# Performance work log

Hardware: AMD Instinct MI355X
Metric: run time of the kernel (lower is better)

Reference implementation:

```python
import jax, jax.numpy as jnp
import numpy as np

N = 20000          # cells (graph nodes)
E = 320000         # edges (avg degree 16)
IN, MID, OUT = 2, 128, 3
HEADS = (4, 4, 1)
CONCAT = (False, False, True)
BN_EPS = 1e-5


def setup_inputs() -> dict:
    key = jax.random.key(0)
    ks = jax.random.split(key, 40)
    f32 = jnp.float32
    inp = {
        "x": jax.random.normal(ks[0], (N, IN), f32),
        "edge_index": jax.random.randint(ks[1], (2, E), 0, N, jnp.int32),
        "gene_index": 0,
    }
    in_dims = (IN, MID, MID)
    out_dims = (MID, MID, OUT)
    i = 2
    for L in range(3):
        H, C = HEADS[L], out_dims[L]
        inp[f"W{L}"] = jax.random.normal(ks[i], (H * C, in_dims[L]), f32) * 0.1; i += 1
        inp[f"as{L}"] = jax.random.normal(ks[i], (H, C), f32) * 0.1; i += 1
        inp[f"ad{L}"] = jax.random.normal(ks[i], (H, C), f32) * 0.1; i += 1
        bdim = H * C if CONCAT[L] else C
        inp[f"b{L}"] = jax.random.normal(ks[i], (bdim,), f32) * 0.1; i += 1
    for L in range(2):
        inp[f"bn_g{L}"] = 1.0 + jax.random.normal(ks[i], (MID,), f32) * 0.1; i += 1
        inp[f"bn_b{L}"] = jax.random.normal(ks[i], (MID,), f32) * 0.1; i += 1
        inp[f"bn_m{L}"] = jax.random.normal(ks[i], (MID,), f32) * 0.1; i += 1
        inp[f"bn_v{L}"] = jax.random.uniform(ks[i], (MID,), f32, minval=0.5, maxval=1.5); i += 1
    inp["k"] = jax.random.normal(ks[i], (1,), f32); i += 1
    inp["d"] = jax.random.normal(ks[i], (1,), f32) * 0.1; i += 1
    inp["t0"] = jax.random.uniform(ks[i], (1,), f32) * 0.2; i += 1
    inp["u0"] = jax.random.uniform(ks[i], (1,), f32); i += 1
    inp["t"] = jax.random.uniform(ks[i], (N, 1), f32); i += 1
    return inp


def _gat(x, W, a_s, a_d, b, src, dst, heads, concat):
    # PyG GATConv (eval): linear -> per-node head scores -> edge leaky_relu
    # -> segment softmax over dst -> scatter-weighted aggregate -> bias.
    n = x.shape[0]
    h = (x @ W.T).reshape(n, heads, -1)                      # [N,H,C]
    logit = jax.nn.leaky_relu(
        (h * a_s).sum(-1)[src] + (h * a_d).sum(-1)[dst], 0.2)  # [E,H]
    m = jax.ops.segment_max(logit, dst, num_segments=n)
    p = jnp.exp(logit - m[dst])
    alpha = p / (jax.ops.segment_sum(p, dst, num_segments=n)[dst] + 1e-16)
    out = jax.ops.segment_sum(h[src] * alpha[:, :, None], dst, num_segments=n)
    out = out.reshape(n, -1) if concat else out.mean(axis=1)
    return out + b


def _forward(x, edge_index, gene_index,
             W0, as0, ad0, b0, W1, as1, ad1, b1, W2, as2, ad2, b2,
             bn_g0, bn_b0, bn_m0, bn_v0, bn_g1, bn_b1, bn_m1, bn_v1,
             k, d, t0, u0, t):
    n = x.shape[0]
    loop = jnp.arange(n, dtype=edge_index.dtype)             # add_self_loops=True
    src = jnp.concatenate([edge_index[0], loop])
    dst = jnp.concatenate([edge_index[1], loop])
    convs = ((W0, as0, ad0, b0), (W1, as1, ad1, b1), (W2, as2, ad2, b2))
    bns = ((bn_g0, bn_b0, bn_m0, bn_v0), (bn_g1, bn_b1, bn_m1, bn_v1))
    for L in range(3):
        W, a_s, a_d, b = convs[L]
        x = jax.nn.elu(_gat(x, W, a_s, a_d, b, src, dst, HEADS[L], CONCAT[L]))
        if L != 2:
            g_, b_, m_, v_ = bns[L]
            x = (x - m_) * jax.lax.rsqrt(v_ + BN_EPS) * g_ + b_   # BN eval
            # dropout is a no-op in eval mode
    a_r = x[:, 0]
    gam = x[:, 1]
    bet = x[:, 2]
    g = gene_index
    tt = t[:, g]
    S = jax.nn.sigmoid(k[g] * (tt - t0[g] - d[g]))
    eb = jnp.exp(-bet * tt)
    eg = jnp.exp(-gam * tt)
    ebs = jnp.exp(-bet * (tt - t0[g]))
    egs = jnp.exp(-gam * (tt - t0[g]))
    ab = a_r / bet
    ag = a_r / gam
    tilde_u = ab * (1 - eb) * (1 - S) + ab * S + (u0[g] * ebs - ab) * S
    tilde_s = (ag * (1 - eg) + a_r / (gam - bet) * (eg - eb)) * (1 - S) \
              + ag * S + bet * u0[g] / (gam - bet) * (egs - ebs) * S
    return tilde_u, tilde_s


def reference(x, edge_index, gene_index,
              W0, as0, ad0, b0, W1, as1, ad1, b1, W2, as2, ad2, b2,
              bn_g0, bn_b0, bn_m0, bn_v0, bn_g1, bn_b1, bn_m1, bn_v1,
              k, d, t0, u0, t):
    return _forward(x, edge_index, gene_index,
                    W0, as0, ad0, b0, W1, as1, ad1, b1, W2, as2, ad2, b2,
                    bn_g0, bn_b0, bn_m0, bn_v0, bn_g1, bn_b1, bn_m1, bn_v1,
                    k, d, t0, u0, t)
```

## Files before the change

### kernel.cpp

```cpp
#include <hip/hip_runtime.h>
#include <hip/hip_bf16.h>

#define CAP 64

typedef __attribute__((ext_vector_type(8))) short bf16x8;
typedef __attribute__((ext_vector_type(4))) float f32x4;

__device__ __forceinline__ float eluf(float x){ return x > 0.f ? x : expm1f(x); }
__device__ __forceinline__ float lrelu(float x){ return x >= 0.f ? x : 0.2f*x; }

__device__ __forceinline__ float ldf(const void* p, size_t i, int f){
  if(f) return ((const float*)p)[i];
  unsigned u = ((const unsigned short*)p)[i];
  return __uint_as_float(u << 16);
}

__device__ __forceinline__ unsigned pk2(float a, float b){
  __hip_bfloat16 ba = __float2bfloat16(a), bb = __float2bfloat16(b);
  unsigned short ua = *(unsigned short*)&ba, ub = *(unsigned short*)&bb;
  return (unsigned)ua | ((unsigned)ub << 16);
}
__device__ __forceinline__ float lo16(unsigned u){ return __uint_as_float(u << 16); }
__device__ __forceinline__ float hi16(unsigned u){ return __uint_as_float(u & 0xffff0000u); }

__device__ __forceinline__ float4 shfl4(float4 v, int m){
  return make_float4(__shfl_xor(v.x,m), __shfl_xor(v.y,m), __shfl_xor(v.z,m), __shfl_xor(v.w,m));
}
__device__ __forceinline__ float4 add4(float4 a, float4 b){
  return make_float4(a.x+b.x, a.y+b.y, a.z+b.z, a.w+b.w);
}

__global__ void zero_detect(const unsigned short* __restrict__ w1raw, int* __restrict__ flag,
                            int* __restrict__ cursor, int N){
  int i = blockIdx.x*256 + threadIdx.x;
  if(i < N) cursor[i] = 0;
  if(blockIdx.x == 0){
    __shared__ int cnt;
    if(threadIdx.x == 0) cnt = 0;
    __syncthreads();
    int c = 0;
    for(int k = threadIdx.x; k < 2048; k += 256){
      unsigned int u = w1raw[2*k];
      float v = __uint_as_float(u << 16);
      if(fabsf(v) > 100.f) c++;
    }
    atomicAdd(&cnt, c);
    __syncthreads();
    if(threadIdx.x == 0) *flag = (cnt > 10) ? 1 : 0;
  }
}

#define NSEG 21
struct CvtDesc {
  const void* src[NSEG];
  float*      dst[NSEG];
  int         n[NSEG];
};
struct POff { int o[26]; };

__global__ void prep(CvtDesc cd, POff po, const int* __restrict__ flag,
    const void* __restrict__ W0r, const void* __restrict__ as0r, const void* __restrict__ ad0r,
    const void* __restrict__ W1r, const void* __restrict__ as1r, const void* __restrict__ ad1r,
    unsigned short* __restrict__ Wgb, float* __restrict__ W1sa, float* __restrict__ W1da,
    float* __restrict__ W0sa, float* __restrict__ W0da,
    const int* __restrict__ ei, int E, int N,
    int* __restrict__ cursor, int* __restrict__ csr){
  int bid = blockIdx.x, t = threadIdx.x;
  int sec = 0;
  while(sec < 24 && bid >= po.o[sec+1]) sec++;
  int lb = bid - po.o[sec];
  int f = *flag;
  if(sec < NSEG){
    int i = lb*256 + t;
    if(i < cd.n[sec]) cd.dst[sec][i] = ldf(cd.src[sec], i, f);
  } else if(sec == NSEG){
    int id = lb*256 + t;
    if(id < 512*128){
      int c = id >> 9, m = id & 511;
      int h = m >> 7, k = m & 127;
      float v = ldf(W1r, (size_t)(h*128 + c)*128 + k, f);
      __hip_bfloat16 bv = __float2bfloat16(v);
      Wgb[id] = *(unsigned short*)&bv;
    }
  } else if(sec == NSEG+1){
    int e = lb*256 + t, Et = E + N;
    if(e < Et){
      int s, d;
      if(e < E){ s = ei[e]; d = ei[E + e]; } else { s = d = e - E; }
      int pos = atomicAdd(&cursor[d], 1);
      if(pos < CAP) csr[(size_t)d*CAP + pos] = s;
    }
  } else if(sec == NSEG+2){
    int gw = (lb*256 + t) >> 6;
    int lane = t & 63;
    int h = gw & 3, w = gw >> 2;
    const void* A = w ? ad1r : as1r;
    float sk0 = 0.f, sk1 = 0.f;
    for(int c = 0; c < 128; c++){
      float a = ldf(A, h*128 + c, f);
      size_t ro = (size_t)(h*128 + c)*128;
      sk0 += ldf(W1r, ro + lane,      f) * a;
      sk1 += ldf(W1r, ro + lane + 64, f) * a;
    }
    float* D = w ? W1da : W1sa;
    D[lane*4 + h]        = sk0;
    D[(lane + 64)*4 + h] = sk1;
  } else {
    int idx = lb*256 + t;
    if(idx < 16){
      int col = idx & 1, h = (idx >> 1) & 3, w = idx >> 3;
      const void* A = w ? ad0r : as0r;
      float s = 0.f;
      for(int c = 0; c < 128; c++)
        s += ldf(W0r, (size_t)(h*128+c)*2 + col, f) * ldf(A, h*128+c, f);
      (w ? W0da : W0sa)[h*2 + col] = s;
    }
  }
}

__global__ __launch_bounds__(256) void gather0(
    const int* __restrict__ cursor, const int* __restrict__ csr,
    const float* __restrict__ xf,
    const float* __restrict__ W0f,
    const float* __restrict__ W0sa, const float* __restrict__ W0da,
    const float* __restrict__ W1sa, const float* __restrict__ W1da,
    const float* __restrict__ b0,
    const float* __restrict__ bn_g, const float* __restrict__ bn_b,
    const float* __restrict__ bn_m, const float* __restrict__ bn_v,
    unsigned* __restrict__ x1b,
    float* __restrict__ ssrc, float* __restrict__ sdst){
  int t = threadIdx.x, wv = t >> 6, lane = t & 63;
  int hh = lane >> 5, l32 = lane & 31;
  int n = blockIdx.x*8 + wv*2 + hh;
  int cnt = min(cursor[n], CAP);
  float2 xn = ((const float2*)xf)[n];
  float4 sd4;
  sd4.x = xn.x*W0da[0] + xn.y*W0da[1];
  sd4.y = xn.x*W0da[2] + xn.y*W0da[3];
  sd4.z = xn.x*W0da[4] + xn.y*W0da[5];
  sd4.w = xn.x*W0da[6] + xn.y*W0da[7];
  float2 xs0 = make_float2(0.f,0.f), xs1 = make_float2(0.f,0.f);
  float4 p0 = make_float4(0.f,0.f,0.f,0.f), p1 = make_float4(0.f,0.f,0.f,0.f);
  if(l32 < cnt){
    int src = csr[(size_t)n*CAP + l32];
    xs0 = ((const float2*)xf)[src];
    p0.x = expf(lrelu(xs0.x*W0sa[0] + xs0.y*W0sa[1] + sd4.x));
    p0.y = expf(lrelu(xs0.x*W0sa[2] + xs0.y*W0sa[3] + sd4.y));
    p0.z = expf(lrelu(xs0.x*W0sa[4] + xs0.y*W0sa[5] + sd4.z));
    p0.w = expf(lrelu(xs0.x*W0sa[6] + xs0.y*W0sa[7] + sd4.w));
  }
  if(l32 + 32 < cnt){
    int src = csr[(size_t)n*CAP + l32 + 32];
    xs1 = ((const float2*)xf)[src];
    p1.x = expf(lrelu(xs1.x*W0sa[0] + xs1.y*W0sa[1] + sd4.x));
    p1.y = expf(lrelu(xs1.x*W0sa[2] + xs1.y*W0sa[3] + sd4.y));
    p1.z = expf(lrelu(xs1.x*W0sa[4] + xs1.y*W0sa[5] + sd4.z));
    p1.w = expf(lrelu(xs1.x*W0sa[6] + xs1.y*W0sa[7] + sd4.w));
  }
  float4 dn = add4(p0, p1);
  #pragma unroll
  for(int o = 1; o < 32; o <<= 1) dn = add4(dn, shfl4(dn, o));
  float4 ax = make_float4(p0.x*xs0.x + p1.x*xs1.x, p0.y*xs0.x + p1.y*xs1.x,
                          p0.z*xs0.x + p1.z*xs1.x, p0.w*xs0.x + p1.w*xs1.x);
  float4 ay = make_float4(p0.x*xs0.y + p1.x*xs1.y, p0.y*xs0.y + p1.y*xs1.y,
                          p0.z*xs0.y + p1.z*xs1.y, p0.w*xs0.y + p1.w*xs1.y);
  #pragma unroll
  for(int o = 1; o < 32; o <<= 1){ ax = add4(ax, shfl4(ax, o)); ay = add4(ay, shfl4(ay, o)); }
  float4 inv;
  inv.x = 1.f/(dn.x + 1e-16f); inv.y = 1.f/(dn.y + 1e-16f);
  inv.z = 1.f/(dn.z + 1e-16f); inv.w = 1.f/(dn.w + 1e-16f);
  ax.x *= inv.x; ax.y *= inv.y; ax.z *= inv.z; ax.w *= inv.w;
  ay.x *= inv.x; ay.y *= inv.y; ay.z *= inv.z; ay.w *= inv.w;
  float o4[4];
  #pragma unroll
  for(int i = 0; i < 4; i++){
    int c = 4*l32 + i;
    float acc = W0f[(c      )*2]*ax.x + W0f[(c      )*2+1]*ay.x
              + W0f[(128 + c)*2]*ax.y + W0f[(128 + c)*2+1]*ay.y
              + W0f[(256 + c)*2]*ax.z + W0f[(256 + c)*2+1]*ay.z
              + W0f[(384 + c)*2]*ax.w + W0f[(384 + c)*2+1]*ay.w;
    float v = 0.25f*acc + b0[c];
    v = eluf(v);
    float sc = bn_g[c] * rsqrtf(bn_v[c] + 1e-5f);
    o4[i] = (v - bn_m[c])*sc + bn_b[c];
  }
  uint2 pk; pk.x = pk2(o4[0], o4[1]); pk.y = pk2(o4[2], o4[3]);
  ((uint2*)(x1b + (size_t)n*64))[l32] = pk;
  float4 ps = make_float4(0.f,0.f,0.f,0.f), pd = make_float4(0.f,0.f,0.f,0.f);
  #pragma unroll
  for(int i = 0; i < 4; i++){
    int c = 4*l32 + i;
    float4 ws = ((const float4*)W1sa)[c];
    float4 wd = ((const float4*)W1da)[c];
    ps.x += o4[i]*ws.x; ps.y += o4[i]*ws.y; ps.z += o4[i]*ws.z; ps.w += o4[i]*ws.w;
    pd.x += o4[i]*wd.x; pd.y += o4[i]*wd.y; pd.z += o4[i]*wd.z; pd.w += o4[i]*wd.w;
  }
  #pragma unroll
  for(int o = 1; o < 32; o <<= 1){ ps = add4(ps, shfl4(ps, o)); pd = add4(pd, shfl4(pd, o)); }
  if(l32 == 0){
    ((float4*)ssrc)[n] = ps;
    ((float4*)sdst)[n] = pd;
  }
}

__global__ __launch_bounds__(256) void agg1(
    const int* __restrict__ cursor, const int* __restrict__ csr,
    const float* __restrict__ s_src, const float* __restrict__ s_dst,
    const unsigned* __restrict__ x1b,
    unsigned* __restrict__ sAgg){
  __shared__ float lal[4][2][CAP*4];
  __shared__ int   lsr[4][2][CAP];
  int t = threadIdx.x, wv = t >> 6, lane = t & 63;
  int hh = lane >> 5, l32 = lane & 31;
  int n = blockIdx.x*8 + wv*2 + hh;
  int cnt = min(cursor[n], CAP);
  float4 sd4 = ((const float4*)s_dst)[n];
  float4 p0 = make_float4(0.f,0.f,0.f,0.f), p1 = make_float4(0.f,0.f,0.f,0.f);
  if(l32 < cnt){
    int src = csr[(size_t)n*CAP + l32];
    lsr[wv][hh][l32] = src;
    float4 ss4 = ((const float4*)s_src)[src];
    p0.x = expf(lrelu(ss4.x + sd4.x)); p0.y = expf(lrelu(ss4.y + sd4.y));
    p0.z = expf(lrelu(ss4.z + sd4.z)); p0.w = expf(lrelu(ss4.w + sd4.w));
    ((float4*)lal[wv][hh])[l32] = p0;
  }
  if(l32 + 32 < cnt){
    int src = csr[(size_t)n*CAP + l32 + 32];
    lsr[wv][hh][l32 + 32] = src;
    float4 ss4 = ((const float4*)s_src)[src];
    p1.x = expf(lrelu(ss4.x + sd4.x)); p1.y = expf(lrelu(ss4.y + sd4.y));
    p1.z = expf(lrelu(ss4.z + sd4.z)); p1.w = expf(lrelu(ss4.w + sd4.w));
    ((float4*)lal[wv][hh])[l32 + 32] = p1;
  }
  float4 dn = add4(p0, p1);
  #pragma unroll
  for(int o = 1; o < 32; o <<= 1) dn = add4(dn, shfl4(dn, o));
  float4 inv;
  inv.x = 1.f/(dn.x + 1e-16f); inv.y = 1.f/(dn.y + 1e-16f);
  inv.z = 1.f/(dn.z + 1e-16f); inv.w = 1.f/(dn.w + 1e-16f);
  float a0[4] = {0,0,0,0}, a1[4] = {0,0,0,0};
  float a2[4] = {0,0,0,0}, a3[4] = {0,0,0,0};
  const float4* alp = (const float4*)lal[wv][hh];
  const int* srcs = lsr[wv][hh];
  #pragma unroll 2
  for(int j = 0; j < cnt; j++){
    int src = srcs[j];
    uint2 uv = ((const uint2*)(x1b + (size_t)src*64))[l32];
    float4 al = alp[j];
    float c0 = lo16(uv.x), c1 = hi16(uv.x);
    float c2 = lo16(uv.y), c3 = hi16(uv.y);
    a0[0] += al.x*c0; a1[0] += al.x*c1; a2[0] += al.x*c2; a3[0] += al.x*c3;
    a0[1] += al.y*c0; a1[1] += al.y*c1; a2[1] += al.y*c2; a3[1] += al.y*c3;
    a0[2] += al.z*c0; a1[2] += al.z*c1; a2[2] += al.z*c2; a3[2] += al.z*c3;
    a0[3] += al.w*c0; a1[3] += al.w*c1; a2[3] += al.w*c2; a3[3] += al.w*c3;
  }
  float iv[4] = {inv.x, inv.y, inv.z, inv.w};
  uint2* out2 = (uint2*)(sAgg + (size_t)n*256);
  #pragma unroll
  for(int h = 0; h < 4; h++){
    uint2 pkv;
    pkv.x = pk2(a0[h]*iv[h], a1[h]*iv[h]);
    pkv.y = pk2(a2[h]*iv[h], a3[h]*iv[h]);
    out2[h*32 + l32] = pkv;
  }
}

__global__ __launch_bounds__(256) void gemm12_mfma(
    const unsigned short* __restrict__ sAgg16,
    const unsigned short* __restrict__ Wgb,
    const float* __restrict__ b1,
    const float* __restrict__ bn_g, const float* __restrict__ bn_b,
    const float* __restrict__ bn_m, const float* __restrict__ bn_v,
    const float* __restrict__ W2f,
    const float* __restrict__ as2f, const float* __restrict__ ad2f,
    float* __restrict__ h2, float* __restrict__ s_src, float* __restrict__ s_dst, int N){
  __shared__ float x2s[64][128];
  int t = threadIdx.x, wv = t >> 6, lane = t & 63;
  int col = lane & 15, quad = lane >> 4;
  int base = blockIdx.x*64;
  const unsigned short* arow = sAgg16 + (size_t)(base + wv*16 + col)*512;
  f32x4 acc[8];
  #pragma unroll
  for(int tc = 0; tc < 8; tc++) acc[tc] = (f32x4){0.f,0.f,0.f,0.f};
  for(int kk = 0; kk < 16; kk++){
    bf16x8 av = *(const bf16x8*)(arow + kk*32 + quad*8);
    #pragma unroll
    for(int tc = 0; tc < 8; tc++){
      bf16x8 bv = *(const bf16x8*)(Wgb + (size_t)(tc*16 + col)*512 + kk*32 + quad*8);
      acc[tc] = __builtin_amdgcn_mfma_f32_16x16x32_bf16(av, bv, acc[tc], 0, 0, 0);
    }
  }
  #pragma unroll
  for(int tc = 0; tc < 8; tc++){
    int ch = tc*16 + col;
    float sc = bn_g[ch] * rsqrtf(bn_v[ch] + 1e-5f);
    float mc = bn_m[ch], ob = bn_b[ch], bb = b1[ch];
    #pragma unroll
    for(int r = 0; r < 4; r++){
      int nl = wv*16 + quad*4 + r;
      float v = eluf(0.25f*acc[tc][r] + bb);
      x2s[nl][ch] = (v - mc)*sc + ob;
    }
  }
  __syncthreads();
  int nd = t >> 2, q = t & 3;
  int n = base + nd;
  const float* xr = x2s[nd];
  float c0 = 0.f, c1 = 0.f, cv2 = 0.f;
  for(int qq = q; qq < 32; qq += 4){
    float4 xv = *(const float4*)&xr[qq*4];
    float4 w0 = ((const float4*)(W2f      ))[qq];
    float4 w1 = ((const float4*)(W2f + 128))[qq];
    float4 w2 = ((const float4*)(W2f + 256))[qq];
    c0  += xv.x*w0.x + xv.y*w0.y + xv.z*w0.z + xv.w*w0.w;
    c1  += xv.x*w1.x + xv.y*w1.y + xv.z*w1.z + xv.w*w1.w;
    cv2 += xv.x*w2.x + xv.y*w2.y + xv.z*w2.z + xv.w*w2.w;
  }
  c0  += __shfl_xor(c0, 1);  c0  += __shfl_xor(c0, 2);
  c1  += __shfl_xor(c1, 1);  c1  += __shfl_xor(c1, 2);
  cv2 += __shfl_xor(cv2, 1); cv2 += __shfl_xor(cv2, 2);
  if(q == 0 && n < N){
    ((float4*)h2)[n] = make_float4(c0, c1, cv2, 0.f);
    s_src[n] = c0*as2f[0] + c1*as2f[1] + cv2*as2f[2];
    s_dst[n] = c0*ad2f[0] + c1*ad2f[1] + cv2*ad2f[2];
  }
}

__global__ __launch_bounds__(256) void gather_ode(const int* __restrict__ cursor,
    const int* __restrict__ csr,
    const float* __restrict__ s_src, const float* __restrict__ s_dst,
    const float* __restrict__ h2, const float* __restrict__ b2f,
    const float* __restrict__ scal,
    const float* __restrict__ tf, float* __restrict__ out, int N){
  int t = threadIdx.x, wv = t >> 6, lane = t & 63;
  int hh = lane >> 5, l32 = lane & 31;
  int n = blockIdx.x*8 + wv*2 + hh;
  int cnt = min(cursor[n], CAP);
  const int* row = csr + (size_t)n*CAP;
  float sd = s_dst[n];
  float pw0 = 0.f, pw1 = 0.f;
  float4 hv0 = make_float4(0,0,0,0), hv1 = make_float4(0,0,0,0);
  if(l32 < cnt){
    int s = row[l32];
    pw0 = expf(lrelu(s_src[s] + sd));
    hv0 = ((const float4*)h2)[s];
  }
  if(l32 + 32 < cnt){
    int s = row[l32 + 32];
    pw1 = expf(lrelu(s_src[s] + sd));
    hv1 = ((const float4*)h2)[s];
  }
  float den = pw0 + pw1;
  float a0 = pw0*hv0.x + pw1*hv1.x;
  float a1 = pw0*hv0.y + pw1*hv1.y;
  float a2 = pw0*hv0.z + pw1*hv1.z;
  #pragma unroll
  for(int o = 1; o < 32; o <<= 1){
    den += __shfl_xor(den, o);
    a0  += __shfl_xor(a0, o);
    a1  += __shfl_xor(a1, o);
    a2  += __shfl_xor(a2, o);
  }
  if(l32 != 0) return;
  double inv = 1.0/((double)den + 1e-16);
  double A0 = (double)a0*inv + (double)b2f[0];
  double A1 = (double)a1*inv + (double)b2f[1];
  double A2 = (double)a2*inv + (double)b2f[2];
  double ar  = A0 > 0.0 ? A0 : expm1(A0);
  double gam = A1 > 0.0 ? A1 : expm1(A1);
  double bet = A2 > 0.0 ? A2 : expm1(A2);
  double tt = (double)tf[n];
  double k = (double)scal[0], d = (double)scal[1];
  double t0 = (double)scal[2], u0 = (double)scal[3];
  double S = 1.0/(1.0 + exp(-(k*(tt - t0 - d))));
  double eb  = exp(-bet*tt),        eg  = exp(-gam*tt);
  double ebs = exp(-bet*(tt - t0)), egs = exp(-gam*(tt - t0));
  double ab = ar/bet, ag = ar/gam;
  double tu = ab*(1.0 - eb)*(1.0 - S) + ab*S + (u0*ebs - ab)*S;
  double gmb = gam - bet;
  double ts = (ag*(1.0 - eg) + ar/gmb*(eg - eb))*(1.0 - S) + ag*S
            + bet*u0/gmb*(egs - ebs)*S;
  out[n]     = (float)tu;
  out[N + n] = (float)ts;
}

extern "C" void kernel_launch(void* const* d_in, const int* in_sizes, int n_in,
                              void* d_out, int out_size, void* d_ws, size_t ws_size,
                              hipStream_t stream) {
  const int* ei = (const int*)d_in[1];
  int N = in_sizes[0] / 2;
  int E = in_sizes[1] / 2;
  int Et = E + N;

  char* ws = (char*)d_ws;
  size_t off = 0;
  auto alloc = [&](size_t bytes)->void*{
    void* p = ws + off; off += (bytes + 255) & ~(size_t)255; return p;
  };
  int*   flag  = (int*)  alloc(4);
  float* xf    = (float*)alloc((size_t)N*2*4);
  float* W0f   = (float*)alloc(1024*4);
  float* b0f   = (float*)alloc(128*4);
  float* b1f   = (float*)alloc(128*4);
  float* W2f   = (float*)alloc(384*4);
  float* as2f  = (float*)alloc(3*4);
  float* ad2f  = (float*)alloc(3*4);
  float* b2f   = (float*)alloc(3*4);
  float* bnf[8];
  for(int i = 0; i < 8; i++) bnf[i] = (float*)alloc(128*4);
  float* scal  = (float*)alloc(4*4);
  float* tf    = (float*)alloc((size_t)N*4);
  unsigned short* Wgb = (unsigned short*)alloc(65536*2);
  float* W1sa  = (float*)alloc(512*4);
  float* W1da  = (float*)alloc(512*4);
  float* W0sa  = (float*)alloc(8*4);
  float* W0da  = (float*)alloc(8*4);
  int*   cursor= (int*)  alloc((size_t)N*4);
  int*   csr   = (int*)  alloc((size_t)N*CAP*4);
  unsigned* x1b= (unsigned*)alloc((size_t)N*64*4);
  unsigned* sAgg=(unsigned*)alloc((size_t)(N + 64)*256*4);
  float* h2    = (float*)alloc((size_t)N*4*4);
  float* ssrc  = (float*)alloc((size_t)N*4*4);
  float* sdst  = (float*)alloc((size_t)N*4*4);

  zero_detect<<<(N + 255)/256, 256, 0, stream>>>((const unsigned short*)d_in[7], flag, cursor, N);

  CvtDesc cd;
  const int src_idx[NSEG] = {0,3,6,10, 11,12,13,14, 15,16,17,18,19,20,21,22, 23,24,25,26, 27};
  float* dsts[NSEG] = {xf,W0f,b0f,b1f, W2f,as2f,ad2f,b2f,
                       bnf[0],bnf[1],bnf[2],bnf[3],bnf[4],bnf[5],bnf[6],bnf[7],
                       scal+0,scal+1,scal+2,scal+3, tf};
  for(int i = 0; i < NSEG; i++){
    cd.src[i] = d_in[src_idx[i]];
    cd.dst[i] = dsts[i];
    cd.n[i]   = in_sizes[src_idx[i]];
  }
  POff po;
  int acc = 0;
  for(int i = 0; i < NSEG; i++){ po.o[i] = acc; acc += (cd.n[i] + 255)/256; }
  po.o[NSEG] = acc;   acc += 256;
  po.o[NSEG+1] = acc; acc += (Et + 255)/256;
  po.o[NSEG+2] = acc; acc += 2;
  po.o[NSEG+3] = acc; acc += 1;
  po.o[NSEG+4] = acc;
  prep<<<acc, 256, 0, stream>>>(cd, po, flag,
      d_in[3], d_in[4], d_in[5], d_in[7], d_in[8], d_in[9],
      Wgb, W1sa, W1da, W0sa, W0da, ei, E, N, cursor, csr);

  gather0<<<N/8, 256, 0, stream>>>(cursor, csr, xf, W0f, W0sa, W0da, W1sa, W1da, b0f,
                                   bnf[0], bnf[1], bnf[2], bnf[3], x1b, ssrc, sdst);
  agg1<<<N/8, 256, 0, stream>>>(cursor, csr, ssrc, sdst, x1b, sAgg);
  gemm12_mfma<<<(N + 63)/64, 256, 0, stream>>>((const unsigned short*)sAgg, Wgb,
                                   b1f, bnf[4], bnf[5], bnf[6], bnf[7],
                                   W2f, as2f, ad2f, h2, ssrc, sdst, N);
  gather_ode<<<N/8, 256, 0, stream>>>(cursor, csr, ssrc, sdst,
                                      h2, b2f, scal, tf,
                                      (float*)d_out, N);
}
```

Before: 247.5 us.

## Fuse all stages into one cooperative persistent kernel with grid syncs

Merges zero/detect, prep, gather0, agg1, gemm12 and gather_ode into a single cooperative kernel that loops over work with grid-stride loops and separates stages with grid-wide syncs. The goal is to remove per-launch overhead and the idle gaps between six dependent launches. The old multi-kernel path stays as a fallback if the cooperative launch fails. In exchange, the grid is capped by occupancy, so the persistent blocks loop over several node groups, and grid syncs carry their own cost. The large union shared buffer may also limit how many blocks fit per CU.

```diff
diff --git a/kernel.cpp b/kernel.cpp
--- a/kernel.cpp
+++ b/kernel.cpp
@@ -1,5 +1,8 @@
 #include <hip/hip_runtime.h>
 #include <hip/hip_bf16.h>
+#include <hip/hip_cooperative_groups.h>
+
+namespace cg = cooperative_groups;
 
 #define CAP 64
 
@@ -28,6 +31,355 @@
 }
 __device__ __forceinline__ float4 add4(float4 a, float4 b){
   return make_float4(a.x+b.x, a.y+b.y, a.z+b.z, a.w+b.w);
+}
+
+#define NSEG 21
+struct CvtDesc {
+  const void* src[NSEG];
+  float*      dst[NSEG];
+  int         n[NSEG];
+};
+struct POff { int o[26]; };
+
+struct MegaArgs {
+  CvtDesc cd; POff po;
+  const unsigned short* w1raw;
+  int* flag; int* cursor; int* csr;
+  const void *W0r, *as0r, *ad0r, *W1r, *as1r, *ad1r;
+  unsigned short* Wgb;
+  float *W1sa, *W1da, *W0sa, *W0da;
+  const int* ei;
+  float *xf, *W0f, *b0f, *b1f, *W2f, *as2f, *ad2f, *b2f;
+  float *bn0g, *bn0b, *bn0m, *bn0v, *bn1g, *bn1b, *bn1m, *bn1v;
+  float *scal, *tf;
+  unsigned *x1b, *sAgg;
+  float *h2, *ssrc, *sdst, *out;
+  int N, E, prep_total;
+};
+
+__global__ __launch_bounds__(256, 4) void mega(MegaArgs a){
+  __shared__ union SM {
+    struct { float lal[4][2][CAP*4]; int lsr[4][2][CAP]; } ag;
+    float x2s[64][128];
+    int cnt;
+  } sm;
+  cg::grid_group gg = cg::this_grid();
+  int t = threadIdx.x, wv = t >> 6, lane = t & 63;
+  int hh = lane >> 5, l32 = lane & 31;
+  int N = a.N, E = a.E;
+
+  for(int i = blockIdx.x*256 + t; i < N; i += gridDim.x*256) a.cursor[i] = 0;
+  if(blockIdx.x == 0){
+    if(t == 0) sm.cnt = 0;
+    __syncthreads();
+    int c = 0;
+    for(int k = t; k < 2048; k += 256){
+      unsigned u = a.w1raw[2*k];
+      float v = __uint_as_float(u << 16);
+      if(fabsf(v) > 100.f) c++;
+    }
+    atomicAdd(&sm.cnt, c);
+    __syncthreads();
+    if(t == 0) *a.flag = (sm.cnt > 10) ? 1 : 0;
+  }
+  gg.sync();
+
+  {
+    int f = *a.flag;
+    for(int vb = blockIdx.x; vb < a.prep_total; vb += gridDim.x){
+      int sec = 0;
+      while(sec < 24 && vb >= a.po.o[sec+1]) sec++;
+      int lb = vb - a.po.o[sec];
+      if(sec < NSEG){
+        int i = lb*256 + t;
+        if(i < a.cd.n[sec]) a.cd.dst[sec][i] = ldf(a.cd.src[sec], i, f);
+      } else if(sec == NSEG){
+        int id = lb*256 + t;
+        if(id < 512*128){
+          int c = id >> 9, m = id & 511;
+          int h = m >> 7, k = m & 127;
+          float v = ldf(a.W1r, (size_t)(h*128 + c)*128 + k, f);
+          __hip_bfloat16 bv = __float2bfloat16(v);
+          a.Wgb[id] = *(unsigned short*)&bv;
+        }
+      } else if(sec == NSEG+1){
+        int e = lb*256 + t, Et = E + N;
+        if(e < Et){
+          int s, d;
+          if(e < E){ s = a.ei[e]; d = a.ei[E + e]; } else { s = d = e - E; }
+          int pos = atomicAdd(&a.cursor[d], 1);
+          if(pos < CAP) a.csr[(size_t)d*CAP + pos] = s;
+        }
+      } else if(sec == NSEG+2){
+        int gw = (lb*256 + t) >> 6;
+        int h = gw & 3, w = gw >> 2;
+        const void* A = w ? a.ad1r : a.as1r;
+        float sk0 = 0.f, sk1 = 0.f;
+        for(int c = 0; c < 128; c++){
+          float av = ldf(A, h*128 + c, f);
+          size_t ro = (size_t)(h*128 + c)*128;
+          sk0 += ldf(a.W1r, ro + lane,      f) * av;
+          sk1 += ldf(a.W1r, ro + lane + 64, f) * av;
+        }
+        float* D = w ? a.W1da : a.W1sa;
+        D[lane*4 + h]        = sk0;
+        D[(lane + 64)*4 + h] = sk1;
+      } else {
+        int idx = lb*256 + t;
+        if(idx < 16){
+          int col = idx & 1, h = (idx >> 1) & 3, w = idx >> 3;
+          const void* A = w ? a.ad0r : a.as0r;
+          float s = 0.f;
+          for(int c = 0; c < 128; c++)
+            s += ldf(a.W0r, (size_t)(h*128+c)*2 + col, f) * ldf(A, h*128+c, f);
+          (w ? a.W0da : a.W0sa)[h*2 + col] = s;
+        }
+      }
+    }
+  }
+  gg.sync();
+
+  for(int nb = blockIdx.x*8; nb < N; nb += gridDim.x*8){
+    int n = nb + wv*2 + hh;
+    int cnt = min(a.cursor[n], CAP);
+    float2 xn = ((const float2*)a.xf)[n];
+    float4 sd4;
+    sd4.x = xn.x*a.W0da[0] + xn.y*a.W0da[1];
+    sd4.y = xn.x*a.W0da[2] + xn.y*a.W0da[3];
+    sd4.z = xn.x*a.W0da[4] + xn.y*a.W0da[5];
+    sd4.w = xn.x*a.W0da[6] + xn.y*a.W0da[7];
+    float2 xs0 = make_float2(0.f,0.f), xs1 = make_float2(0.f,0.f);
+    float4 p0 = make_float4(0.f,0.f,0.f,0.f), p1 = make_float4(0.f,0.f,0.f,0.f);
+    if(l32 < cnt){
+      int src = a.csr[(size_t)n*CAP + l32];
+      xs0 = ((const float2*)a.xf)[src];
+      p0.x = expf(lrelu(xs0.x*a.W0sa[0] + xs0.y*a.W0sa[1] + sd4.x));
+      p0.y = expf(lrelu(xs0.x*a.W0sa[2] + xs0.y*a.W0sa[3] + sd4.y));
+      p0.z = expf(lrelu(xs0.x*a.W0sa[4] + xs0.y*a.W0sa[5] + sd4.z));
+      p0.w = expf(lrelu(xs0.x*a.W0sa[6] + xs0.y*a.W0sa[7] + sd4.w));
+    }
+    if(l32 + 32 < cnt){
+      int src = a.csr[(size_t)n*CAP + l32 + 32];
+      xs1 = ((const float2*)a.xf)[src];
+      p1.x = expf(lrelu(xs1.x*a.W0sa[0] + xs1.y*a.W0sa[1] + sd4.x));
+      p1.y = expf(lrelu(xs1.x*a.W0sa[2] + xs1.y*a.W0sa[3] + sd4.y));
+      p1.z = expf(lrelu(xs1.x*a.W0sa[4] + xs1.y*a.W0sa[5] + sd4.z));
+      p1.w = expf(lrelu(xs1.x*a.W0sa[6] + xs1.y*a.W0sa[7] + sd4.w));
+    }
+    float4 dn = add4(p0, p1);
+    #pragma unroll
+    for(int o = 1; o < 32; o <<= 1) dn = add4(dn, shfl4(dn, o));
+    float4 ax = make_float4(p0.x*xs0.x + p1.x*xs1.x, p0.y*xs0.x + p1.y*xs1.x,
+                            p0.z*xs0.x + p1.z*xs1.x, p0.w*xs0.x + p1.w*xs1.x);
+    float4 ay = make_float4(p0.x*xs0.y + p1.x*xs1.y, p0.y*xs0.y + p1.y*xs1.y,
+                            p0.z*xs0.y + p1.z*xs1.y, p0.w*xs0.y + p1.w*xs1.y);
+    #pragma unroll
+    for(int o = 1; o < 32; o <<= 1){ ax = add4(ax, shfl4(ax, o)); ay = add4(ay, shfl4(ay, o)); }
+    float4 inv;
+    inv.x = 1.f/(dn.x + 1e-16f); inv.y = 1.f/(dn.y + 1e-16f);
+    inv.z = 1.f/(dn.z + 1e-16f); inv.w = 1.f/(dn.w + 1e-16f);
+    ax.x *= inv.x; ax.y *= inv.y; ax.z *= inv.z; ax.w *= inv.w;
+    ay.x *= inv.x; ay.y *= inv.y; ay.z *= inv.z; ay.w *= inv.w;
+    float o4[4];
+    #pragma unroll
+    for(int i = 0; i < 4; i++){
+      int c = 4*l32 + i;
+      float acc = a.W0f[(c      )*2]*ax.x + a.W0f[(c      )*2+1]*ay.x
+                + a.W0f[(128 + c)*2]*ax.y + a.W0f[(128 + c)*2+1]*ay.y
+                + a.W0f[(256 + c)*2]*ax.z + a.W0f[(256 + c)*2+1]*ay.z
+                + a.W0f[(384 + c)*2]*ax.w + a.W0f[(384 + c)*2+1]*ay.w;
+      float v = 0.25f*acc + a.b0f[c];
+      v = eluf(v);
+      float sc = a.bn0g[c] * rsqrtf(a.bn0v[c] + 1e-5f);
+      o4[i] = (v - a.bn0m[c])*sc + a.bn0b[c];
+    }
+    uint2 pk; pk.x = pk2(o4[0], o4[1]); pk.y = pk2(o4[2], o4[3]);
+    ((uint2*)(a.x1b + (size_t)n*64))[l32] = pk;
+    float4 ps = make_float4(0.f,0.f,0.f,0.f), pd = make_float4(0.f,0.f,0.f,0.f);
+    #pragma unroll
+    for(int i = 0; i < 4; i++){
+      int c = 4*l32 + i;
+      float4 ws = ((const float4*)a.W1sa)[c];
+      float4 wd = ((const float4*)a.W1da)[c];
+      ps.x += o4[i]*ws.x; ps.y += o4[i]*ws.y; ps.z += o4[i]*ws.z; ps.w += o4[i]*ws.w;
+      pd.x += o4[i]*wd.x; pd.y += o4[i]*wd.y; pd.z += o4[i]*wd.z; pd.w += o4[i]*wd.w;
+    }
+    #pragma unroll
+    for(int o = 1; o < 32; o <<= 1){ ps = add4(ps, shfl4(ps, o)); pd = add4(pd, shfl4(pd, o)); }
+    if(l32 == 0){
+      ((float4*)a.ssrc)[n] = ps;
+      ((float4*)a.sdst)[n] = pd;
+    }
+  }
+  gg.sync();
+
+  for(int nb = blockIdx.x*8; nb < N; nb += gridDim.x*8){
+    int n = nb + wv*2 + hh;
+    int cnt = min(a.cursor[n], CAP);
+    float4 sd4 = ((const float4*)a.sdst)[n];
+    float4 p0 = make_float4(0.f,0.f,0.f,0.f), p1 = make_float4(0.f,0.f,0.f,0.f);
+    if(l32 < cnt){
+      int src = a.csr[(size_t)n*CAP + l32];
+      sm.ag.lsr[wv][hh][l32] = src;
+      float4 ss4 = ((const float4*)a.ssrc)[src];
+      p0.x = expf(lrelu(ss4.x + sd4.x)); p0.y = expf(lrelu(ss4.y + sd4.y));
+      p0.z = expf(lrelu(ss4.z + sd4.z)); p0.w = expf(lrelu(ss4.w + sd4.w));
+      ((float4*)sm.ag.lal[wv][hh])[l32] = p0;
+    }
+    if(l32 + 32 < cnt){
+      int src = a.csr[(size_t)n*CAP + l32 + 32];
+      sm.ag.lsr[wv][hh][l32 + 32] = src;
+      float4 ss4 = ((const float4*)a.ssrc)[src];
+      p1.x = expf(lrelu(ss4.x + sd4.x)); p1.y = expf(lrelu(ss4.y + sd4.y));
+      p1.z = expf(lrelu(ss4.z + sd4.z)); p1.w = expf(lrelu(ss4.w + sd4.w));
+      ((float4*)sm.ag.lal[wv][hh])[l32 + 32] = p1;
+    }
+    float4 dn = add4(p0, p1);
+    #pragma unroll
+    for(int o = 1; o < 32; o <<= 1) dn = add4(dn, shfl4(dn, o));
+    float4 inv;
+    inv.x = 1.f/(dn.x + 1e-16f); inv.y = 1.f/(dn.y + 1e-16f);
+    inv.z = 1.f/(dn.z + 1e-16f); inv.w = 1.f/(dn.w + 1e-16f);
+    float a0[4] = {0,0,0,0}, a1[4] = {0,0,0,0};
+    float a2[4] = {0,0,0,0}, a3[4] = {0,0,0,0};
+    const float4* alp = (const float4*)sm.ag.lal[wv][hh];
+    const int* srcs = sm.ag.lsr[wv][hh];
+    #pragma unroll 2
+    for(int j = 0; j < cnt; j++){
+      int src = srcs[j];
+      uint2 uv = ((const uint2*)(a.x1b + (size_t)src*64))[l32];
+      float4 al = alp[j];
+      float c0 = lo16(uv.x), c1 = hi16(uv.x);
+      float c2 = lo16(uv.y), c3 = hi16(uv.y);
+      a0[0] += al.x*c0; a1[0] += al.x*c1; a2[0] += al.x*c2; a3[0] += al.x*c3;
+      a0[1] += al.y*c0; a1[1] += al.y*c1; a2[1] += al.y*c2; a3[1] += al.y*c3;
+      a0[2] += al.z*c0; a1[2] += al.z*c1; a2[2] += al.z*c2; a3[2] += al.z*c3;
+      a0[3] += al.w*c0; a1[3] += al.w*c1; a2[3] += al.w*c2; a3[3] += al.w*c3;
+    }
+    float iv[4] = {inv.x, inv.y, inv.z, inv.w};
+    uint2* out2 = (uint2*)(a.sAgg + (size_t)n*256);
+    #pragma unroll
+    for(int h = 0; h < 4; h++){
+      uint2 pkv;
+      pkv.x = pk2(a0[h]*iv[h], a1[h]*iv[h]);
+      pkv.y = pk2(a2[h]*iv[h], a3[h]*iv[h]);
+      out2[h*32 + l32] = pkv;
+    }
+  }
+  gg.sync();
+
+  {
+    int col = lane & 15, quad = lane >> 4;
+    int ntile = (N + 63) >> 6;
+    const unsigned short* sAgg16 = (const unsigned short*)a.sAgg;
+    for(int tile = blockIdx.x; tile < ntile; tile += gridDim.x){
+      int base = tile*64;
+      const unsigned short* arow = sAgg16 + (size_t)(base + wv*16 + col)*512;
+      #pragma unroll 1
+      for(int hu = 0; hu < 2; hu++){
+        f32x4 acc[4];
+        #pragma unroll
+        for(int tc = 0; tc < 4; tc++) acc[tc] = (f32x4){0.f,0.f,0.f,0.f};
+        for(int kk = 0; kk < 16; kk++){
+          bf16x8 av = *(const bf16x8*)(arow + kk*32 + quad*8);
+          #pragma unroll
+          for(int tc = 0; tc < 4; tc++){
+            int tcg = hu*4 + tc;
+            bf16x8 bv = *(const bf16x8*)(a.Wgb + (size_t)(tcg*16 + col)*512 + kk*32 + quad*8);
+            acc[tc] = __builtin_amdgcn_mfma_f32_16x16x32_bf16(av, bv, acc[tc], 0, 0, 0);
+          }
+        }
+        #pragma unroll
+        for(int tc = 0; tc < 4; tc++){
+          int ch = (hu*4 + tc)*16 + col;
+          float sc = a.bn1g[ch] * rsqrtf(a.bn1v[ch] + 1e-5f);
+          float mc = a.bn1m[ch], ob = a.bn1b[ch], bb = a.b1f[ch];
+          #pragma unroll
+          for(int r = 0; r < 4; r++){
+            int nl = wv*16 + quad*4 + r;
+            float v = eluf(0.25f*acc[tc][r] + bb);
+            sm.x2s[nl][ch] = (v - mc)*sc + ob;
+          }
+        }
+      }
+      __syncthreads();
+      int nd = t >> 2, q = t & 3;
+      int n2 = base + nd;
+      const float* xr = sm.x2s[nd];
+      float c0 = 0.f, c1 = 0.f, cv2 = 0.f;
+      for(int qq = q; qq < 32; qq += 4){
+        float4 xv = *(const float4*)&xr[qq*4];
+        float4 w0 = ((const float4*)(a.W2f      ))[qq];
+        float4 w1 = ((const float4*)(a.W2f + 128))[qq];
+        float4 w2 = ((const float4*)(a.W2f + 256))[qq];
+        c0  += xv.x*w0.x + xv.y*w0.y + xv.z*w0.z + xv.w*w0.w;
+        c1  += xv.x*w1.x + xv.y*w1.y + xv.z*w1.z + xv.w*w1.w;
+        cv2 += xv.x*w2.x + xv.y*w2.y + xv.z*w2.z + xv.w*w2.w;
+      }
+      c0  += __shfl_xor(c0, 1);  c0  += __shfl_xor(c0, 2);
+      c1  += __shfl_xor(c1, 1);  c1  += __shfl_xor(c1, 2);
+      cv2 += __shfl_xor(cv2, 1); cv2 += __shfl_xor(cv2, 2);
+      if(q == 0 && n2 < N){
+        ((float4*)a.h2)[n2] = make_float4(c0, c1, cv2, 0.f);
+        a.ssrc[n2] = c0*a.as2f[0] + c1*a.as2f[1] + cv2*a.as2f[2];
+        a.sdst[n2] = c0*a.ad2f[0] + c1*a.ad2f[1] + cv2*a.ad2f[2];
+      }
+      __syncthreads();
+    }
+  }
+  gg.sync();
+
+  for(int nb = blockIdx.x*8; nb < N; nb += gridDim.x*8){
+    int n = nb + wv*2 + hh;
+    int cnt = min(a.cursor[n], CAP);
+    const int* row = a.csr + (size_t)n*CAP;
+    float sd = a.sdst[n];
+    float pw0 = 0.f, pw1 = 0.f;
+    float4 hv0 = make_float4(0,0,0,0), hv1 = make_float4(0,0,0,0);
+    if(l32 < cnt){
+      int s = row[l32];
+      pw0 = expf(lrelu(a.ssrc[s] + sd));
+      hv0 = ((const float4*)a.h2)[s];
+    }
+    if(l32 + 32 < cnt){
+      int s = row[l32 + 32];
+      pw1 = expf(lrelu(a.ssrc[s] + sd));
+      hv1 = ((const float4*)a.h2)[s];
+    }
+    float den = pw0 + pw1;
+    float a0 = pw0*hv0.x + pw1*hv1.x;
+    float a1 = pw0*hv0.y + pw1*hv1.y;
+    float a2 = pw0*hv0.z + pw1*hv1.z;
+    #pragma unroll
+    for(int o = 1; o < 32; o <<= 1){
+      den += __shfl_xor(den, o);
+      a0  += __shfl_xor(a0, o);
+      a1  += __shfl_xor(a1, o);
+      a2  += __shfl_xor(a2, o);
+    }
+    if(l32 == 0){
+      double inv = 1.0/((double)den + 1e-16);
+      double A0 = (double)a0*inv + (double)a.b2f[0];
+      double A1 = (double)a1*inv + (double)a.b2f[1];
+      double A2 = (double)a2*inv + (double)a.b2f[2];
+      double ar  = A0 > 0.0 ? A0 : expm1(A0);
+      double gam = A1 > 0.0 ? A1 : expm1(A1);
+      double bet = A2 > 0.0 ? A2 : expm1(A2);
+      double tt = (double)a.tf[n];
+      double k = (double)a.scal[0], d = (double)a.scal[1];
+      double t0 = (double)a.scal[2], u0 = (double)a.scal[3];
+      double S = 1.0/(1.0 + exp(-(k*(tt - t0 - d))));
+      double eb  = exp(-bet*tt),        eg  = exp(-gam*tt);
+      double ebs = exp(-bet*(tt - t0)), egs = exp(-gam*(tt - t0));
+      double ab = ar/bet, ag = ar/gam;
+      double tu = ab*(1.0 - eb)*(1.0 - S) + ab*S + (u0*ebs - ab)*S;
+      double gmb = gam - bet;
+      double ts = (ag*(1.0 - eg) + ar/gmb*(eg - eb))*(1.0 - S) + ag*S
+                + bet*u0/gmb*(egs - ebs)*S;
+      a.out[n]       = (float)tu;
+      a.out[N + n]   = (float)ts;
+    }
+  }
 }
 
 __global__ void zero_detect(const unsigned short* __restrict__ w1raw, int* __restrict__ flag,
@@ -49,14 +401,6 @@
     if(threadIdx.x == 0) *flag = (cnt > 10) ? 1 : 0;
   }
 }
-
-#define NSEG 21
-struct CvtDesc {
-  const void* src[NSEG];
-  float*      dst[NSEG];
-  int         n[NSEG];
-};
-struct POff { int o[26]; };
 
 __global__ void prep(CvtDesc cd, POff po, const int* __restrict__ flag,
     const void* __restrict__ W0r, const void* __restrict__ as0r, const void* __restrict__ ad0r,
@@ -97,10 +441,10 @@
     const void* A = w ? ad1r : as1r;
     float sk0 = 0.f, sk1 = 0.f;
     for(int c = 0; c < 128; c++){
-      float a = ldf(A, h*128 + c, f);
+      float av = ldf(A, h*128 + c, f);
       size_t ro = (size_t)(h*128 + c)*128;
-      sk0 += ldf(W1r, ro + lane,      f) * a;
-      sk1 += ldf(W1r, ro + lane + 64, f) * a;
+      sk0 += ldf(W1r, ro + lane,      f) * av;
+      sk1 += ldf(W1r, ro + lane + 64, f) * av;
     }
     float* D = w ? W1da : W1sa;
     D[lane*4 + h]        = sk0;
@@ -423,8 +767,6 @@
   float* ssrc  = (float*)alloc((size_t)N*4*4);
   float* sdst  = (float*)alloc((size_t)N*4*4);
 
-  zero_detect<<<(N + 255)/256, 256, 0, stream>>>((const unsigned short*)d_in[7], flag, cursor, N);
-
   CvtDesc cd;
   const int src_idx[NSEG] = {0,3,6,10, 11,12,13,14, 15,16,17,18,19,20,21,22, 23,24,25,26, 27};
   float* dsts[NSEG] = {xf,W0f,b0f,b1f, W2f,as2f,ad2f,b2f,
@@ -443,17 +785,48 @@
   po.o[NSEG+2] = acc; acc += 2;
   po.o[NSEG+3] = acc; acc += 1;
   po.o[NSEG+4] = acc;
-  prep<<<acc, 256, 0, stream>>>(cd, po, flag,
-      d_in[3], d_in[4], d_in[5], d_in[7], d_in[8], d_in[9],
-      Wgb, W1sa, W1da, W0sa, W0da, ei, E, N, cursor, csr);
-
-  gather0<<<N/8, 256, 0, stream>>>(cursor, csr, xf, W0f, W0sa, W0da, W1sa, W1da, b0f,
-                                   bnf[0], bnf[1], bnf[2], bnf[3], x1b, ssrc, sdst);
-  agg1<<<N/8, 256, 0, stream>>>(cursor, csr, ssrc, sdst, x1b, sAgg);
-  gemm12_mfma<<<(N + 63)/64, 256, 0, stream>>>((const unsigned short*)sAgg, Wgb,
-                                   b1f, bnf[4], bnf[5], bnf[6], bnf[7],
-                                   W2f, as2f, ad2f, h2, ssrc, sdst, N);
-  gather_ode<<<N/8, 256, 0, stream>>>(cursor, csr, ssrc, sdst,
-                                      h2, b2f, scal, tf,
-                                      (float*)d_out, N);
-}
+
+  bool coop_ok = false;
+  int occ = 0;
+  hipError_t oe = hipOccupancyMaxActiveBlocksPerMultiprocessor(&occ, mega, 256, 0);
+  if(oe == hipSuccess && occ > 0){
+    int grid = occ * 256;
+    if(grid > 2500) grid = 2500;
+    MegaArgs ma;
+    ma.cd = cd; ma.po = po;
+    ma.w1raw = (const unsigned short*)d_in[7];
+    ma.flag = flag; ma.cursor = cursor; ma.csr = csr;
+    ma.W0r = d_in[3]; ma.as0r = d_in[4]; ma.ad0r = d_in[5];
+    ma.W1r = d_in[7]; ma.as1r = d_in[8]; ma.ad1r = d_in[9];
+    ma.Wgb = Wgb; ma.W1sa = W1sa; ma.W1da = W1da; ma.W0sa = W0sa; ma.W0da = W0da;
+    ma.ei = ei;
+    ma.xf = xf; ma.W0f = W0f; ma.b0f = b0f; ma.b1f = b1f; ma.W2f = W2f;
+    ma.as2f = as2f; ma.ad2f = ad2f; ma.b2f = b2f;
+    ma.bn0g = bnf[0]; ma.bn0b = bnf[1]; ma.bn0m = bnf[2]; ma.bn0v = bnf[3];
+    ma.bn1g = bnf[4]; ma.bn1b = bnf[5]; ma.bn1m = bnf[6]; ma.bn1v = bnf[7];
+    ma.scal = scal; ma.tf = tf;
+    ma.x1b = x1b; ma.sAgg = sAgg;
+    ma.h2 = h2; ma.ssrc = ssrc; ma.sdst = sdst;
+    ma.out = (float*)d_out;
+    ma.N = N; ma.E = E; ma.prep_total = acc;
+    void* kp[] = { (void*)&ma };
+    if(hipLaunchCooperativeKernel(mega, dim3(grid), dim3(256), kp, 0, stream) == hipSuccess)
+      coop_ok = true;
+  }
+
+  if(!coop_ok){
+    zero_detect<<<(N + 255)/256, 256, 0, stream>>>((const unsigned short*)d_in[7], flag, cursor, N);
+    prep<<<acc, 256, 0, stream>>>(cd, po, flag,
+        d_in[3], d_in[4], d_in[5], d_in[7], d_in[8], d_in[9],
+        Wgb, W1sa, W1da, W0sa, W0da, ei, E, N, cursor, csr);
+    gather0<<<N/8, 256, 0, stream>>>(cursor, csr, xf, W0f, W0sa, W0da, W1sa, W1da, b0f,
+                                     bnf[0], bnf[1], bnf[2], bnf[3], x1b, ssrc, sdst);
+    agg1<<<N/8, 256, 0, stream>>>(cursor, csr, ssrc, sdst, x1b, sAgg);
+    gemm12_mfma<<<(N + 63)/64, 256, 0, stream>>>((const unsigned short*)sAgg, Wgb,
+                                     b1f, bnf[4], bnf[5], bnf[6], bnf[7],
+                                     W2f, as2f, ad2f, h2, ssrc, sdst, N);
+    gather_ode<<<N/8, 256, 0, stream>>>(cursor, csr, ssrc, sdst,
+                                        h2, b2f, scal, tf,
+                                        (float*)d_out, N);
+  }
+}
```

After: 595.3 us. 2.41x slower.
